# Kernel optimization log

Measured on AMD Instinct MI355X. Metric: run time of the kernel, lower is better.

The kernel has to match this reference:

```python
import jax, jax.numpy as jnp
import numpy as np

C = 256
B, H, W = 16, 64, 64
CQK = C // 8


def setup_inputs() -> dict:
    key = jax.random.key(0)
    ks = jax.random.split(key, 8)
    s = 0.02
    return {
        "x": jax.random.normal(ks[0], (B, C, H, W), dtype=jnp.float32),
        "Wq": jax.random.normal(ks[1], (CQK, C), dtype=jnp.float32) * s,
        "bq": jax.random.normal(ks[2], (CQK,), dtype=jnp.float32) * s,
        "Wk": jax.random.normal(ks[3], (CQK, C), dtype=jnp.float32) * s,
        "bk": jax.random.normal(ks[4], (CQK,), dtype=jnp.float32) * s,
        "Wv": jax.random.normal(ks[5], (C, C), dtype=jnp.float32) * s,
        "bv": jax.random.normal(ks[6], (C,), dtype=jnp.float32) * s,
        "gamma": jax.random.normal(ks[7], (1,), dtype=jnp.float32) * 0.1,
    }


def reference(x, Wq, bq, Wk, bk, Wv, bv, gamma):
    b, c, h, w = x.shape
    n = h * w
    xf = x.reshape(b, c, n)  # flatten spatial -> tokens
    # 1x1 convs are per-token linear maps over channels
    q = jnp.einsum('oc,bcn->bon', Wq, xf) + bq[None, :, None]  # [B, C/8, N]
    k = jnp.einsum('oc,bcn->bon', Wk, xf) + bk[None, :, None]  # [B, C/8, N]
    v = jnp.einsum('oc,bcn->bon', Wv, xf) + bv[None, :, None]  # [B, C,   N]
    attn = jnp.einsum('bdi,bdj->bij', q, k)        # [B, N, N] = Q^T K
    attn = jax.nn.softmax(attn, axis=2)            # softmax over keys
    out = jnp.einsum('bcj,bij->bci', v, attn)      # V @ attn^T -> [B, C, N]
    out = out.reshape(b, c, h, w)
    return gamma[0] * out + x
```

## Files before the change

### kernel.cpp

```cpp
#include <hip/hip_runtime.h>
#include <hip/hip_bf16.h>

#define BB   16
#define CCH  256
#define DQK  32
#define NTOK 4096

typedef __attribute__((ext_vector_type(8)))  short short8;
typedef __attribute__((ext_vector_type(4)))  float f32x4;
typedef __attribute__((ext_vector_type(16))) float f32x16;
typedef unsigned short u16t;
typedef unsigned int   u32t;
typedef long long      i64t;

__device__ __forceinline__ u16t f2bf(float f){
  u32t u = __builtin_bit_cast(u32t, f);
  u += 0x7FFFu + ((u >> 16) & 1u);
  return (u16t)(u >> 16);
}
__device__ __forceinline__ u32t pk2(float a, float b){
  return (u32t)f2bf(a) | ((u32t)f2bf(b) << 16);
}
__device__ __forceinline__ void lane32swap(u32t& a, u32t& b){
  asm("v_permlane32_swap_b32 %0, %1" : "+v"(a), "+v"(b));
}
__device__ __forceinline__ float swapadd(float x){
  u32t a = __builtin_bit_cast(u32t, x), b = a;
  lane32swap(a, b);
  return __builtin_bit_cast(float, a) + __builtin_bit_cast(float, b);
}
__device__ __forceinline__ void gload16(const void* g, void* l){
  __builtin_amdgcn_global_load_lds(
      (const __attribute__((address_space(1))) void*)g,
      (__attribute__((address_space(3))) void*)l, 16, 0, 0);
}
__device__ __forceinline__ f32x16 zero16(){
  f32x16 z;
  #pragma unroll
  for (int i = 0; i < 16; ++i) z[i] = 0.f;
  return z;
}
#define mfma32(A, B, C)  __builtin_amdgcn_mfma_f32_32x32x16_bf16((A), (B), (C), 0, 0, 0)
#define mfma8(A, B, C)   __builtin_amdgcn_mfma_f32_32x32x16_fp8_fp8((A), (B), (C), 0, 0, 0)
__device__ __forceinline__ u32t pack4fp8(float a, float b, float c, float d){
  int t = __builtin_amdgcn_cvt_pk_fp8_f32(a, b, 0, false);
  t = __builtin_amdgcn_cvt_pk_fp8_f32(c, d, t, true);
  return (u32t)t;
}
__device__ __forceinline__ unsigned char tofp8(float v){
  return (unsigned char)(__builtin_amdgcn_cvt_pk_fp8_f32(v, 0.f, 0, false) & 0xFF);
}

__global__ __launch_bounds__(256) void k_wconv(const float* __restrict__ Wq,
    const float* __restrict__ Wk, const float* __restrict__ Wv,
    u16t* __restrict__ o){
  const int base = (blockIdx.x * 256 + threadIdx.x) * 4;
  float4 v;
  if (base < 8192)        v = *(const float4*)(Wq + base);
  else if (base < 16384)  v = *(const float4*)(Wk + base - 8192);
  else                    v = *(const float4*)(Wv + base - 16384);
  *(uint2*)(o + base) = make_uint2(pk2(v.x, v.y), pk2(v.z, v.w));
}

__global__ __launch_bounds__(256) void k_proj(const float* __restrict__ x,
    const u16t* __restrict__ Wb,
    const float* __restrict__ bq, const float* __restrict__ bk,
    const float* __restrict__ bv,
    u16t* __restrict__ Q, u16t* __restrict__ K, unsigned char* __restrict__ V){
  __shared__ __align__(16) u16t xt[32 * 512];
  const int b = blockIdx.y, nb = blockIdx.x * 64;
  const int tid = threadIdx.x;
  const int w = tid >> 6, lane = tid & 63;
  const int lo = lane & 15, g = lane >> 4;

  const float* xb = x + (size_t)b * CCH * NTOK + nb;
  const int cg = tid >> 4, n0 = (tid & 15) * 4;
  #pragma unroll
  for (int rep = 0; rep < 16; ++rep){
    const int c = rep * 16 + cg;
    float4 v = *(const float4*)(xb + (size_t)c * NTOK + n0);
    const int chunkb = (n0 >> 4) * 8 + (c >> 5);
    const int fl = 16 * ((c >> 3) & 3);
    const int e = c & 7;
    xt[chunkb * 512 + ((n0 & 15) + 0 + fl) * 8 + e] = f2bf(v.x);
    xt[chunkb * 512 + ((n0 & 15) + 1 + fl) * 8 + e] = f2bf(v.y);
    xt[chunkb * 512 + ((n0 & 15) + 2 + fl) * 8 + e] = f2bf(v.z);
    xt[chunkb * 512 + ((n0 & 15) + 3 + fl) * 8 + e] = f2bf(v.w);
  }
  __syncthreads();

  #pragma unroll
  for (int ot = 0; ot < 5; ++ot){
    const u16t* Wrow; const float* bias; int ob; int mode;
    if (ot == 0){
      if (w < 2){ Wrow = Wb;        bias = bq; ob = w * 16;       mode = 0; }
      else      { Wrow = Wb + 8192; bias = bk; ob = (w - 2) * 16; mode = 1; }
    } else { Wrow = Wb + 16384; bias = bv; ob = (ot - 1) * 64 + w * 16; mode = 2; }
    const u16t* wp = Wrow + (size_t)(ob + lo) * CCH + g * 8;

    f32x4 acc[4];
    #pragma unroll
    for (int s = 0; s < 4; ++s) acc[s] = (f32x4){0.f, 0.f, 0.f, 0.f};
    #pragma unroll
    for (int kc = 0; kc < CCH; kc += 32){
      const short8 af = *(const short8*)(wp + kc);
      #pragma unroll
      for (int s = 0; s < 4; ++s){
        const short8 bf = *(const short8*)(xt + (s * 8 + (kc >> 5)) * 512 + lane * 8);
        acc[s] = __builtin_amdgcn_mfma_f32_16x16x32_bf16(af, bf, acc[s], 0, 0, 0);
      }
    }
    #pragma unroll
    for (int s = 0; s < 4; ++s){
      #pragma unroll
      for (int r = 0; r < 4; ++r){
        const int o = ob + 4 * g + r;
        const int n = nb + s * 16 + lo;
        float val = acc[s][r] + bias[o];
        if (mode == 0){
          val *= 1.44269504088896f;
          Q[((size_t)b * NTOK + n) * DQK + o] = f2bf(val);
        } else if (mode == 1){
          K[((size_t)b * NTOK + n) * DQK + o] = f2bf(val);
        } else {
          const int swz = ((((s * 2) + (lo >> 3)) ^ ((o >> 1) & 7)) << 3) + (lo & 7);
          V[((size_t)b * CCH + o) * (size_t)NTOK + nb + swz] = tofp8(val);
        }
      }
    }
  }
}

__global__ __launch_bounds__(512, 4) void k_attn(
    const u16t* __restrict__ Q, const u16t* __restrict__ K,
    const unsigned char* __restrict__ V,
    const float* __restrict__ x, const float* __restrict__ gamma,
    float* __restrict__ out){
  __shared__ __align__(16) u16t KT[2 * 2048];
  __shared__ __align__(16) unsigned char Vt[2][16384];
  const int bid = blockIdx.x;
  const int b  = ((bid & 7) << 1) | ((bid >> 3) & 1);
  const int qt = bid >> 4;
  const int tid = threadIdx.x, w = tid >> 6, lane = tid & 63;
  const int qg = w & 3, ch = w >> 2;
  const int ql = lane & 31, hi = lane >> 5;
  const int qgb = qt * 128 + qg * 32;

  const u16t* Qb = Q + (size_t)b * NTOK * DQK;
  const u16t* Kb = K + (size_t)b * NTOK * DQK;
  const unsigned char* Vb = V + (size_t)b * CCH * NTOK;

  const short8 qf0 = *(const short8*)(Qb + (size_t)(qgb + ql) * DQK + hi * 8);
  const short8 qf1 = *(const short8*)(Qb + (size_t)(qgb + ql) * DQK + 16 + hi * 8);

  f32x16 acc[4];
  #pragma unroll
  for (int c = 0; c < 4; ++c) acc[c] = zero16();
  float l = 0.f;

  const char* vsrc0 = (const char*)Vb + (size_t)(w * 32 + (lane >> 2)) * NTOK + (lane & 3) * 16;
  const size_t kse = (size_t)((w & 1) * 32 + ql) * DQK + (w >> 1) * 16 + hi * 8;
  const char* ksrc0 = (const char*)Kb + kse * 2;
  const int kla = lane * 16;
  int vadd[4];
  #pragma unroll
  for (int kt = 0; kt < 4; ++kt)
    vadd[kt] = (ch * 128 + ql) * 64 + (((kt * 2 + hi) ^ ((ql >> 1) & 7)) << 3);
  const char* ldsV = (const char*)&Vt[0][0];
  const char* ldsK = (const char*)&KT[0];
  u32t pf2[4][2];

  #define PACK_PF8(S0, S1) \
    { _Pragma("unroll") \
      for (int kt_ = 0; kt_ < 4; ++kt_){ \
        const int bo = (kt_ & 1) * 8; \
        u32t A, B; \
        if (kt_ < 2){ \
          A = pack4fp8(S0[bo+0], S0[bo+1], S0[bo+2], S0[bo+3]); \
          B = pack4fp8(S0[bo+4], S0[bo+5], S0[bo+6], S0[bo+7]); \
        } else { \
          A = pack4fp8(S1[bo+0], S1[bo+1], S1[bo+2], S1[bo+3]); \
          B = pack4fp8(S1[bo+4], S1[bo+5], S1[bo+6], S1[bo+7]); \
        } \
        lane32swap(A, B); \
        pf2[kt_][0] = A; pf2[kt_][1] = B; \
      } }

  #define QK_STEP(KRD, S0, S1) \
    { const char* kb_ = ldsK + (KRD) * 4096; \
      const short8 kf00 = *(const short8*)(kb_ + kla + 0 * 1024); \
      const short8 kf10 = *(const short8*)(kb_ + kla + 1 * 1024); \
      const short8 kf01 = *(const short8*)(kb_ + kla + 2 * 1024); \
      const short8 kf11 = *(const short8*)(kb_ + kla + 3 * 1024); \
      S0 = mfma32(kf00, qf0, zero16()); S0 = mfma32(kf01, qf1, S0); \
      S1 = mfma32(kf10, qf0, zero16()); S1 = mfma32(kf11, qf1, S1); }

  #define ESL(S, B) \
    { S[(B)+0] = __builtin_amdgcn_exp2f(S[(B)+0]); r0 += S[(B)+0]; \
      S[(B)+1] = __builtin_amdgcn_exp2f(S[(B)+1]); r1 += S[(B)+1]; \
      S[(B)+2] = __builtin_amdgcn_exp2f(S[(B)+2]); r2 += S[(B)+2]; \
      S[(B)+3] = __builtin_amdgcn_exp2f(S[(B)+3]); r3 += S[(B)+3]; }

  #define PVCHUNK(CS, VRD, EXPSLICE) \
    { const i64t vf0 = *(const i64t*)(ldsV + vadd[0] + (VRD)*16384 + (CS)*2048); \
      const i64t vf1 = *(const i64t*)(ldsV + vadd[1] + (VRD)*16384 + (CS)*2048); \
      const i64t vf2 = *(const i64t*)(ldsV + vadd[2] + (VRD)*16384 + (CS)*2048); \
      const i64t vf3 = *(const i64t*)(ldsV + vadd[3] + (VRD)*16384 + (CS)*2048); \
      acc[CS] = mfma8(vf0, pb0, acc[CS]); \
      acc[CS] = mfma8(vf1, pb1, acc[CS]); \
      acc[CS] = mfma8(vf2, pb2, acc[CS]); \
      acc[CS] = mfma8(vf3, pb3, acc[CS]); \
      EXPSLICE \
      __builtin_amdgcn_sched_group_barrier(0x100, 4, 0); \
      __builtin_amdgcn_sched_group_barrier(0x8,   4, 0); \
      __builtin_amdgcn_sched_group_barrier(0x2,  16, 0); }

  #define NOSL
  #define PBDEFS \
      const i64t pb0 = __builtin_bit_cast(i64t, make_uint2(pf2[0][0], pf2[0][1])); \
      const i64t pb1 = __builtin_bit_cast(i64t, make_uint2(pf2[1][0], pf2[1][1])); \
      const i64t pb2 = __builtin_bit_cast(i64t, make_uint2(pf2[2][0], pf2[2][1])); \
      const i64t pb3 = __builtin_bit_cast(i64t, make_uint2(pf2[3][0], pf2[3][1]));

  #define ABODY(T, VRD, KRD, KST) { \
      const int toff_ = ((T) + 1) * 64; \
      _Pragma("unroll") \
      for (int i = 0; i < 2; ++i) \
        gload16(vsrc0 + (size_t)i * 16 * NTOK + toff_, &Vt[(VRD)^1][w * 2048 + i * 1024]); \
      if (w < 4){ const int kt2_ = ((T) + 2 <= 63) ? (T) + 2 : 63; \
        gload16(ksrc0 + (size_t)kt2_ * 4096, &KT[(KST) * 2048 + w * 512]); } \
      f32x16 s0, s1; \
      QK_STEP(KRD, s0, s1); \
      PBDEFS \
      float r0 = 0.f, r1 = 0.f, r2 = 0.f, r3 = 0.f; \
      PVCHUNK(0, VRD, ESL(s0, 0) ESL(s0, 4)) \
      PVCHUNK(1, VRD, ESL(s0, 8) ESL(s0, 12)) \
      PVCHUNK(2, VRD, ESL(s1, 0) ESL(s1, 4)) \
      PVCHUNK(3, VRD, ESL(s1, 8) ESL(s1, 12)) \
      l += (r0 + r1) + (r2 + r3); \
      PACK_PF8(s0, s1); \
      __syncthreads(); }

  #pragma unroll
  for (int i = 0; i < 2; ++i)
    gload16(vsrc0 + (size_t)i * 16 * NTOK, &Vt[0][w * 2048 + i * 1024]);
  if (w < 4){
    gload16(ksrc0,        &KT[0 * 2048 + w * 512]);
    gload16(ksrc0 + 4096, &KT[1 * 2048 + w * 512]);
  }
  __syncthreads();

  {
    f32x16 s0, s1;
    QK_STEP(0, s0, s1);
    float r0 = 0.f, r1 = 0.f, r2 = 0.f, r3 = 0.f;
    ESL(s0, 0) ESL(s0, 4) ESL(s0, 8) ESL(s0, 12)
    ESL(s1, 0) ESL(s1, 4) ESL(s1, 8) ESL(s1, 12)
    l = (r0 + r1) + (r2 + r3);
    PACK_PF8(s0, s1);
  }
  __syncthreads();

  for (int t = 0; t < 62; t += 2){
    ABODY(t,     0, 1, 0)
    ABODY(t + 1, 1, 0, 1)
  }
  ABODY(62, 0, 1, 0)

  {
    PBDEFS
    PVCHUNK(0, 1, NOSL) PVCHUNK(1, 1, NOSL)
    PVCHUNK(2, 1, NOSL) PVCHUNK(3, 1, NOSL)
  }

  const float lfull = swapadd(l);
  const float inv = 1.0f / lfull;
  const float gm = gamma[0];
  const int n = qgb + ql;
  #pragma unroll
  for (int cs = 0; cs < 4; ++cs){
    #pragma unroll
    for (int r = 0; r < 16; ++r){
      const int c = ch * 128 + cs * 32 + (r & 3) + 8 * (r >> 2) + 4 * hi;
      const size_t idx = ((size_t)b * CCH + c) * NTOK + n;
      out[idx] = gm * (acc[cs][r] * inv) + x[idx];
    }
  }
  #undef PACK_PF8
  #undef QK_STEP
  #undef ESL
  #undef PVCHUNK
  #undef NOSL
  #undef PBDEFS
  #undef ABODY
}

extern "C" void kernel_launch(void* const* d_in, const int* in_sizes, int n_in,
                              void* d_out, int out_size, void* d_ws, size_t ws_size,
                              hipStream_t stream) {
  const float* x     = (const float*)d_in[0];
  const float* Wq    = (const float*)d_in[1];
  const float* bq    = (const float*)d_in[2];
  const float* Wk    = (const float*)d_in[3];
  const float* bk    = (const float*)d_in[4];
  const float* Wv    = (const float*)d_in[5];
  const float* bv    = (const float*)d_in[6];
  const float* gamma = (const float*)d_in[7];
  float* out = (float*)d_out;

  char* ws = (char*)d_ws;
  u16t* Qw = (u16t*)(ws);
  u16t* Kw = (u16t*)(ws + 4194304);
  unsigned char* Vw = (unsigned char*)(ws + 8388608);
  u16t* Wbf = (u16t*)d_out;

  hipLaunchKernelGGL(k_wconv, dim3(80), dim3(256), 0, stream, Wq, Wk, Wv, Wbf);
  hipLaunchKernelGGL(k_proj, dim3(NTOK / 64, BB), dim3(256), 0, stream,
                     x, Wbf, bq, bk, bv, Qw, Kw, Vw);
  hipLaunchKernelGGL(k_attn, dim3(512), dim3(512), 0, stream,
                     Qw, Kw, Vw, x, gamma, out);
}
```

Baseline: 199.9 us.

## Split QK^T scores between channel-half waves and share P tiles via LDS

Before, both channel-half waves in a query group each computed the full 64-key score tile, so QK^T MFMA and exp work was duplicated. Now each wave computes half of the keys (32), exponentiates them, packs them to fp8 and writes them into a double-buffered shared-memory P tile. Both waves then read the full P operand from LDS for the PV MFMAs. The row sums are combined across the two waves through shared memory at the end. This removes redundant exp and MFMA work at the cost of extra LDS traffic, 16KB more shared memory and a dependency on the barrier between writing and reading P.

```diff
diff --git a/kernel.cpp b/kernel.cpp
--- a/kernel.cpp
+++ b/kernel.cpp
@@ -138,6 +138,7 @@
     float* __restrict__ out){
   __shared__ __align__(16) u16t KT[2 * 2048];
   __shared__ __align__(16) unsigned char Vt[2][16384];
+  __shared__ __align__(16) unsigned char PT[2][8192];
   const int bid = blockIdx.x;
   const int b  = ((bid & 7) << 1) | ((bid >> 3) & 1);
   const int qt = bid >> 4;
@@ -168,32 +169,8 @@
     vadd[kt] = (ch * 128 + ql) * 64 + (((kt * 2 + hi) ^ ((ql >> 1) & 7)) << 3);
   const char* ldsV = (const char*)&Vt[0][0];
   const char* ldsK = (const char*)&KT[0];
-  u32t pf2[4][2];
-
-  #define PACK_PF8(S0, S1) \
-    { _Pragma("unroll") \
-      for (int kt_ = 0; kt_ < 4; ++kt_){ \
-        const int bo = (kt_ & 1) * 8; \
-        u32t A, B; \
-        if (kt_ < 2){ \
-          A = pack4fp8(S0[bo+0], S0[bo+1], S0[bo+2], S0[bo+3]); \
-          B = pack4fp8(S0[bo+4], S0[bo+5], S0[bo+6], S0[bo+7]); \
-        } else { \
-          A = pack4fp8(S1[bo+0], S1[bo+1], S1[bo+2], S1[bo+3]); \
-          B = pack4fp8(S1[bo+4], S1[bo+5], S1[bo+6], S1[bo+7]); \
-        } \
-        lane32swap(A, B); \
-        pf2[kt_][0] = A; pf2[kt_][1] = B; \
-      } }
-
-  #define QK_STEP(KRD, S0, S1) \
-    { const char* kb_ = ldsK + (KRD) * 4096; \
-      const short8 kf00 = *(const short8*)(kb_ + kla + 0 * 1024); \
-      const short8 kf10 = *(const short8*)(kb_ + kla + 1 * 1024); \
-      const short8 kf01 = *(const short8*)(kb_ + kla + 2 * 1024); \
-      const short8 kf11 = *(const short8*)(kb_ + kla + 3 * 1024); \
-      S0 = mfma32(kf00, qf0, zero16()); S0 = mfma32(kf01, qf1, S0); \
-      S1 = mfma32(kf10, qf0, zero16()); S1 = mfma32(kf11, qf1, S1); }
+  const char* ldsP = (const char*)&PT[0][0];
+  char* ldsPw = (char*)&PT[0][0] + qg * 2048 + (ch * 2) * 512 + lane * 8;
 
   #define ESL(S, B) \
     { S[(B)+0] = __builtin_amdgcn_exp2f(S[(B)+0]); r0 += S[(B)+0]; \
@@ -213,37 +190,52 @@
       EXPSLICE \
       __builtin_amdgcn_sched_group_barrier(0x100, 4, 0); \
       __builtin_amdgcn_sched_group_barrier(0x8,   4, 0); \
-      __builtin_amdgcn_sched_group_barrier(0x2,  16, 0); }
+      __builtin_amdgcn_sched_group_barrier(0x2,   8, 0); }
 
   #define NOSL
-  #define PBDEFS \
-      const i64t pb0 = __builtin_bit_cast(i64t, make_uint2(pf2[0][0], pf2[0][1])); \
-      const i64t pb1 = __builtin_bit_cast(i64t, make_uint2(pf2[1][0], pf2[1][1])); \
-      const i64t pb2 = __builtin_bit_cast(i64t, make_uint2(pf2[2][0], pf2[2][1])); \
-      const i64t pb3 = __builtin_bit_cast(i64t, make_uint2(pf2[3][0], pf2[3][1]));
+  #define PBREADS(VRD) \
+      const i64t pb0 = *(const i64t*)(ldsP + (VRD)*8192 + qg*2048 + 0*512 + lane*8); \
+      const i64t pb1 = *(const i64t*)(ldsP + (VRD)*8192 + qg*2048 + 1*512 + lane*8); \
+      const i64t pb2 = *(const i64t*)(ldsP + (VRD)*8192 + qg*2048 + 2*512 + lane*8); \
+      const i64t pb3 = *(const i64t*)(ldsP + (VRD)*8192 + qg*2048 + 3*512 + lane*8);
+
+  #define QKH(KRD, S) \
+      { const char* kb_ = ldsK + (KRD)*4096 + ch*1024 + kla; \
+        const short8 kfA = *(const short8*)(kb_); \
+        const short8 kfB = *(const short8*)(kb_ + 2048); \
+        S = mfma32(kfA, qf0, zero16()); \
+        S = mfma32(kfB, qf1, S); }
+
+  #define PWRITE(S, WB) \
+      { u32t A1 = pack4fp8(S[0], S[1], S[2],  S[3]); \
+        u32t B1 = pack4fp8(S[4], S[5], S[6],  S[7]); \
+        lane32swap(A1, B1); \
+        u32t A2 = pack4fp8(S[8], S[9], S[10], S[11]); \
+        u32t B2 = pack4fp8(S[12], S[13], S[14], S[15]); \
+        lane32swap(A2, B2); \
+        *(i64t*)(ldsPw + (WB)*8192)       = __builtin_bit_cast(i64t, make_uint2(A1, B1)); \
+        *(i64t*)(ldsPw + (WB)*8192 + 512) = __builtin_bit_cast(i64t, make_uint2(A2, B2)); }
 
   #define ABODY(T, VRD, KRD, KST) { \
       const int toff_ = ((T) + 1) * 64; \
-      _Pragma("unroll") \
-      for (int i = 0; i < 2; ++i) \
-        gload16(vsrc0 + (size_t)i * 16 * NTOK + toff_, &Vt[(VRD)^1][w * 2048 + i * 1024]); \
+      gload16(vsrc0 + toff_,                     &Vt[(VRD)^1][w * 2048]); \
+      gload16(vsrc0 + (size_t)16 * NTOK + toff_, &Vt[(VRD)^1][w * 2048 + 1024]); \
       if (w < 4){ const int kt2_ = ((T) + 2 <= 63) ? (T) + 2 : 63; \
         gload16(ksrc0 + (size_t)kt2_ * 4096, &KT[(KST) * 2048 + w * 512]); } \
-      f32x16 s0, s1; \
-      QK_STEP(KRD, s0, s1); \
-      PBDEFS \
+      PBREADS(VRD) \
+      f32x16 s; \
+      QKH(KRD, s) \
       float r0 = 0.f, r1 = 0.f, r2 = 0.f, r3 = 0.f; \
-      PVCHUNK(0, VRD, ESL(s0, 0) ESL(s0, 4)) \
-      PVCHUNK(1, VRD, ESL(s0, 8) ESL(s0, 12)) \
-      PVCHUNK(2, VRD, ESL(s1, 0) ESL(s1, 4)) \
-      PVCHUNK(3, VRD, ESL(s1, 8) ESL(s1, 12)) \
+      PVCHUNK(0, VRD, ESL(s, 0)) \
+      PVCHUNK(1, VRD, ESL(s, 4)) \
+      PVCHUNK(2, VRD, ESL(s, 8)) \
+      PVCHUNK(3, VRD, ESL(s, 12)) \
       l += (r0 + r1) + (r2 + r3); \
-      PACK_PF8(s0, s1); \
+      PWRITE(s, (VRD)^1) \
       __syncthreads(); }
 
-  #pragma unroll
-  for (int i = 0; i < 2; ++i)
-    gload16(vsrc0 + (size_t)i * 16 * NTOK, &Vt[0][w * 2048 + i * 1024]);
+  gload16(vsrc0,                     &Vt[0][w * 2048]);
+  gload16(vsrc0 + (size_t)16 * NTOK, &Vt[0][w * 2048 + 1024]);
   if (w < 4){
     gload16(ksrc0,        &KT[0 * 2048 + w * 512]);
     gload16(ksrc0 + 4096, &KT[1 * 2048 + w * 512]);
@@ -251,13 +243,12 @@
   __syncthreads();
 
   {
-    f32x16 s0, s1;
-    QK_STEP(0, s0, s1);
+    f32x16 s;
+    QKH(0, s)
     float r0 = 0.f, r1 = 0.f, r2 = 0.f, r3 = 0.f;
-    ESL(s0, 0) ESL(s0, 4) ESL(s0, 8) ESL(s0, 12)
-    ESL(s1, 0) ESL(s1, 4) ESL(s1, 8) ESL(s1, 12)
+    ESL(s, 0) ESL(s, 4) ESL(s, 8) ESL(s, 12)
     l = (r0 + r1) + (r2 + r3);
-    PACK_PF8(s0, s1);
+    PWRITE(s, 0)
   }
   __syncthreads();
 
@@ -268,12 +259,17 @@
   ABODY(62, 0, 1, 0)
 
   {
-    PBDEFS
+    PBREADS(1)
     PVCHUNK(0, 1, NOSL) PVCHUNK(1, 1, NOSL)
     PVCHUNK(2, 1, NOSL) PVCHUNK(3, 1, NOSL)
   }
 
-  const float lfull = swapadd(l);
+  __syncthreads();
+  const float lhalf = swapadd(l);
+  float* lx = (float*)&PT[0][0];
+  if (lane < 32) lx[(qg * 2 + ch) * 32 + ql] = lhalf;
+  __syncthreads();
+  const float lfull = lhalf + lx[(qg * 2 + (ch ^ 1)) * 32 + ql];
   const float inv = 1.0f / lfull;
   const float gm = gamma[0];
   const int n = qgb + ql;
@@ -286,12 +282,12 @@
       out[idx] = gm * (acc[cs][r] * inv) + x[idx];
     }
   }
-  #undef PACK_PF8
-  #undef QK_STEP
   #undef ESL
   #undef PVCHUNK
   #undef NOSL
-  #undef PBDEFS
+  #undef PBREADS
+  #undef QKH
+  #undef PWRITE
   #undef ABODY
 }
 
```

After: 163.6 us. 1.22x faster.
